# Kernel tuning notes

Measured on AMD Instinct MI355X. Metric: run time of the kernel, lower is better.

The kernel has to match this reference:

```python
import jax, jax.numpy as jnp
import numpy as np

B, C, H, W = 2, 64, 256, 256
DW = 128          # c * DW_Expand
FFN = 128         # c * FFN_Expand
GRID = 8          # wH = wW modulation grid


def setup_inputs() -> dict:
    key = jax.random.key(0)
    ks = jax.random.split(key, 16)
    rn = lambda k, s, sc=1.0: jax.random.normal(k, s, jnp.float32) * sc
    return {
        "x": rn(ks[0], (B, C, H, W)),
        "w1": rn(ks[1], (DW, C), (2.0 / C) ** 0.5),
        "b1": jnp.zeros((DW,), jnp.float32),
        "w2": rn(ks[2], (DW, 3, 3), (2.0 / 9.0) ** 0.5),
        "b2": jnp.zeros((DW,), jnp.float32),
        "w3": rn(ks[3], (C, DW // 2), (2.0 / (DW // 2)) ** 0.5),
        "b3": jnp.zeros((C,), jnp.float32),
        "sca_w": rn(ks[4], (DW // 2, DW // 2), (1.0 / (DW // 2)) ** 0.5),
        "sca_b": jnp.zeros((DW // 2,), jnp.float32),
        "w4": rn(ks[5], (FFN, C), (2.0 / C) ** 0.5),
        "b4": jnp.zeros((FFN,), jnp.float32),
        "w5": rn(ks[6], (C, FFN // 2), (2.0 / (FFN // 2)) ** 0.5),
        "b5": jnp.zeros((C,), jnp.float32),
        "n1_w": jnp.ones((C,), jnp.float32),
        "n1_b": jnp.zeros((C,), jnp.float32),
        "n2_w": jnp.ones((C,), jnp.float32),
        "n2_b": jnp.zeros((C,), jnp.float32),
        "beta": rn(ks[7], (C,), 0.1),
        "gamma": rn(ks[8], (C,), 0.1),
        "mod1": rn(ks[9], (B, DW, C, GRID, GRID)),
        "mod2": rn(ks[10], (B, DW, GRID, GRID)),
        "mod3": rn(ks[11], (B, C, DW // 2, GRID, GRID)),
        "mod4": rn(ks[12], (B, FFN, C, GRID, GRID)),
        "mod5": rn(ks[13], (B, C, FFN // 2, GRID, GRID)),
    }


def layernorm2d(x, w, b, eps=1e-6):
    # channel-wise LayerNorm per pixel (NAFNet LayerNorm2d)
    mu = jnp.mean(x, axis=1, keepdims=True)
    var = jnp.mean((x - mu) ** 2, axis=1, keepdims=True)
    return (x - mu) / jnp.sqrt(var + eps) * w[None, :, None, None] + b[None, :, None, None]


def conv1x1_modulated(x, wb, bb, mod):
    # wb: [Co,Ci], mod: [B,Co,Ci,wH,wW]; per-patch 1x1 conv with normalized dynamic weights
    w = wb[None, :, :, None, None] * mod                      # [B,Co,Ci,wH,wW]
    w = w / jnp.sqrt(jnp.sum(w * w, axis=2, keepdims=True))   # normalize over Ci (kh*kw==1)
    b_, ci, h, wd = x.shape
    wh, ww = mod.shape[-2:]
    ph, pw = h // wh, wd // ww
    xp = x.reshape(b_, ci, wh, ph, ww, pw)                    # split into patches
    y = jnp.einsum('bocuv,bcupvq->boupvq', w, xp)             # per-patch matmul
    return y.reshape(b_, wb.shape[0], h, wd) + bb[None, :, None, None]


def conv3x3_dw_modulated(x, wb, bb, mod):
    # wb: [C,3,3], mod: [B,C,wH,wW]; per-patch depthwise 3x3, padding 1 across whole image
    w = wb[None, :, :, :, None, None] * mod[:, :, None, None, :, :]  # [B,C,3,3,wH,wW]
    w = w / jnp.sqrt(jnp.sum(w * w, axis=(2, 3), keepdims=True))     # normalize over (ci=1, kh*kw)
    b_, c, h, wd = x.shape
    wh, ww = mod.shape[-2:]
    ph, pw = h // wh, wd // ww
    xpad = jnp.pad(x, ((0, 0), (0, 0), (1, 1), (1, 1)))
    out = jnp.zeros_like(x)
    for dh in range(3):
        for dw_ in range(3):
            xs = xpad[:, :, dh:dh + h, dw_:dw_ + wd].reshape(b_, c, wh, ph, ww, pw)
            wk = w[:, :, dh, dw_, :, :]                        # [B,C,wH,wW]
            out = out + (wk[:, :, :, None, :, None] * xs).reshape(b_, c, h, wd)
    return out + bb[None, :, None, None]


def simple_gate(x):
    a, g = jnp.split(x, 2, axis=1)
    return a * g


def reference(x, w1, b1, w2, b2, w3, b3, sca_w, sca_b, w4, b4, w5, b5,
              n1_w, n1_b, n2_w, n2_b, beta, gamma, mod1, mod2, mod3, mod4, mod5):
    y = layernorm2d(x, n1_w, n1_b)
    y = conv1x1_modulated(y, w1, b1, mod1)
    y = conv3x3_dw_modulated(y, w2, b2, mod2)
    y = simple_gate(y)
    s = jnp.mean(y, axis=(2, 3), keepdims=True)               # SCA: global pool + 1x1
    s = jnp.einsum('oc,bcij->boij', sca_w, s) + sca_b[None, :, None, None]
    y = y * s
    y = conv1x1_modulated(y, w3, b3, mod3)
    y1 = x + y * beta[None, :, None, None]
    z = conv1x1_modulated(layernorm2d(y1, n2_w, n2_b), w4, b4, mod4)
    z = simple_gate(z)
    z = conv1x1_modulated(z, w5, b5, mod5)
    return y1 + z * gamma[None, :, None, None]
```

## Files before the change

kernel.cpp:

```cpp
#include <hip/hip_runtime.h>


typedef __bf16 bf16x8 __attribute__((ext_vector_type(8)));
typedef float f32x4 __attribute__((ext_vector_type(4)));
typedef unsigned short u16x8 __attribute__((ext_vector_type(8)));

__device__ __forceinline__ float b2f(unsigned short u) {
    union { unsigned int i; float f; } x; x.i = ((unsigned int)u) << 16; return x.f;
}
__device__ __forceinline__ unsigned short f2b(float f) {
    union { float f; unsigned int i; } x; x.f = f;
    unsigned int i = x.i;
    return (unsigned short)((i + 0x7FFFu + ((i >> 16) & 1u)) >> 16);
}

__global__ __launch_bounds__(256) void prep_k(
    const float* __restrict__ w1, const float* __restrict__ mod1,
    const float* __restrict__ w3, const float* __restrict__ mod3,
    const float* __restrict__ beta,
    const float* __restrict__ w4, const float* __restrict__ mod4,
    unsigned short* __restrict__ pw1, unsigned short* __restrict__ pw3,
    unsigned short* __restrict__ pw4)
{
    const int tid = threadIdx.x;
    int blk = blockIdx.x;
    const float* w; const float* mod; const float* rows = nullptr;
    unsigned short* out; int NOUT; int rem;
    if (blk < 256)      { w = w1; mod = mod1; out = pw1; NOUT = 128; rem = blk; }
    else if (blk < 384) { w = w3; mod = mod3; out = pw3; NOUT = 64; rem = blk - 256; rows = beta; }
    else                { w = w4; mod = mod4; out = pw4; NOUT = 128; rem = blk - 384; }
    const int b = rem / NOUT, o = rem % NOUT;

    __shared__ float mlds[64 * 68];
    __shared__ float wlsh[64];
    __shared__ float red[4 * 64];
    __shared__ float rs[64];

    const float* mbase = mod + ((size_t)(b * NOUT + o) * 64) * 64;
#pragma unroll
    for (int k = 0; k < 4; ++k) {
        int l = tid + k * 256;
        float4 vv = ((const float4*)mbase)[l];
        int c = l >> 4, q = l & 15;
        *(float4*)&mlds[c * 68 + q * 4] = vv;
    }
    if (tid < 64) wlsh[tid] = w[o * 64 + tid];
    __syncthreads();

    {
        int uv = tid & 63, part = tid >> 6;
        float ss = 0.f;
#pragma unroll
        for (int j = 0; j < 16; ++j) {
            int c = part * 16 + j;
            float t = wlsh[c] * mlds[c * 68 + uv];
            ss += t * t;
        }
        red[part * 64 + uv] = ss;
    }
    __syncthreads();
    if (tid < 64) {
        float tot = red[tid] + red[64 + tid] + red[128 + tid] + red[192 + tid];
        float rv = rows ? rows[o] : 1.f;
        rs[tid] = rsqrtf(fmaxf(tot, 1e-30f)) * rv;
    }
    __syncthreads();

    {
        int uvw = tid >> 2, cp = tid & 3;
        float r = rs[uvw];
        size_t obase = ((size_t)(b * 64 + uvw) * NOUT + o) * 64;
#pragma unroll
        for (int g = 0; g < 2; ++g) {
            u16x8 pk;
#pragma unroll
            for (int e = 0; e < 8; ++e) {
                int c = cp * 16 + g * 8 + e;
                pk[e] = f2b(wlsh[c] * mlds[c * 68 + uvw] * r);
            }
            *(u16x8*)&out[obase + cp * 16 + g * 8] = pk;
        }
    }
}

template <int NOUT, bool LN, bool GATE, bool RESID, bool SCALE_IN,
          bool IN_F32, bool RES_F32, bool OUT_F32, bool PREPPED>
__global__ __launch_bounds__(256, 2) void conv_k(
    const void* __restrict__ in_,
    void* __restrict__ out_,
    const unsigned short* __restrict__ pw,
    const float* __restrict__ wb,
    const float* __restrict__ mod,
    const float* __restrict__ bias,
    const float* __restrict__ lnw,
    const float* __restrict__ lnb,
    const void* __restrict__ resid_,
    const float* __restrict__ rows,
    const float* __restrict__ svec,
    int bbase)
{
    constexpr int CHOUT = GATE ? 64 : NOUT;
    constexpr int PARTS = 256 / NOUT;
    constexpr int CP    = 64 / PARTS;

    const int tid   = threadIdx.x;
    const int chunk = blockIdx.x;
    const int uv    = blockIdx.y;
    const int z     = blockIdx.z;
    const int bfull = z + bbase;
    const int u = uv >> 3, v = uv & 7;
    const int h_base = u * 32 + chunk * 4;
    const int w_base = v * 32;

    __shared__ __align__(16) unsigned short stage[128 * 72];
    __shared__ __align__(16) unsigned short wlds[NOUT * 72];
    __shared__ float sbias[NOUT];
    __shared__ float shP[PREPPED ? 1 : 256];
    __shared__ float shsA[LN ? 256 : 1];
    __shared__ float shsB[LN ? 256 : 1];

    const int o_p  = tid & (NOUT - 1);
    const int part = tid / NOUT;
    float wv[PREPPED ? 1 : CP];

    if constexpr (PREPPED) {
        constexpr int CH = NOUT / 32;
        const unsigned short* pwb = pw + ((size_t)(bfull * 64 + uv) * NOUT) * 64;
#pragma unroll
        for (int k = 0; k < CH; ++k) {
            int ci = tid + k * 256;
            *(u16x8*)&wlds[(ci >> 3) * 72 + (ci & 7) * 8] = *(const u16x8*)&pwb[ci * 8];
        }
        if (tid < NOUT) {
            float bs = bias[tid];
            if constexpr (RESID) bs *= rows[tid];
            sbias[tid] = bs;
        }
    } else {
        float ss = 0.f;
#pragma unroll
        for (int j = 0; j < CP; ++j) {
            int c = part * CP + j;
            float wf = wb[o_p * 64 + c];
            float m  = mod[(((bfull * NOUT + o_p) * 64 + c) << 6) + uv];
            wv[j] = wf * m;
            ss += wv[j] * wv[j];
        }
        shP[o_p * PARTS + part] = ss;
    }

    const int p    = tid & 127;
    const int half = tid >> 7;
    const int cbase = half * 32;
    const int pixoff = (h_base + (p >> 5)) * 256 + w_base + (p & 31);
    float v2[32];
    {
        float s1 = 0.f, s2 = 0.f;
#pragma unroll
        for (int j = 0; j < 32; ++j) {
            int idx = ((z * 64 + cbase + j) << 16) + pixoff;
            float xv = IN_F32 ? ((const float*)in_)[idx]
                              : b2f(((const unsigned short*)in_)[idx]);
            v2[j] = xv;
            if constexpr (LN) { s1 += xv; s2 += xv * xv; }
        }
        if constexpr (LN) { shsA[p * 2 + half] = s1; shsB[p * 2 + half] = s2; }
    }

    if constexpr (!LN) {
#pragma unroll
        for (int g = 0; g < 4; ++g) {
            u16x8 pk;
#pragma unroll
            for (int e = 0; e < 8; ++e) {
                int j = g * 8 + e;
                float val = v2[j];
                if constexpr (SCALE_IN) val *= svec[bfull * 64 + cbase + j];
                pk[e] = f2b(val);
            }
            *(u16x8*)&stage[p * 72 + cbase + g * 8] = pk;
        }
    }

    if constexpr (LN || !PREPPED) __syncthreads();

    if constexpr (!PREPPED) {
        float tot = 0.f;
#pragma unroll
        for (int k = 0; k < PARTS; ++k) tot += shP[o_p * PARTS + k];
        float rn = rsqrtf(fmaxf(tot, 1e-30f));
        float rsv = 1.f;
        if constexpr (RESID) { rsv = rows[o_p]; rn *= rsv; }
#pragma unroll
        for (int j = 0; j < CP; ++j)
            wlds[o_p * 72 + part * CP + j] = f2b(wv[j] * rn);
        if (part == 0) {
            float bs = bias[o_p];
            if constexpr (RESID) bs *= rsv;
            sbias[o_p] = bs;
        }
    }

    if constexpr (LN) {
        float S1 = shsA[p * 2] + shsA[p * 2 + 1];
        float S2 = shsB[p * 2] + shsB[p * 2 + 1];
        float mu = S1 * (1.f / 64.f);
        float var = S2 * (1.f / 64.f) - mu * mu;
        float rstd = rsqrtf(fmaxf(var, 0.f) + 1e-6f);
#pragma unroll
        for (int g = 0; g < 4; ++g) {
            u16x8 pk;
#pragma unroll
            for (int e = 0; e < 8; ++e) {
                int j = g * 8 + e;
                float val = (v2[j] - mu) * rstd * lnw[cbase + j] + lnb[cbase + j];
                pk[e] = f2b(val);
            }
            *(u16x8*)&stage[p * 72 + cbase + g * 8] = pk;
        }
    }

    __syncthreads();

    const int wave = tid >> 6;
    const int lane = tid & 63;
    const int q = lane >> 4;
    const int r = lane & 15;

    constexpr int NF = (NOUT == 64) ? 1 : 2;
    int nfi[2];
    if constexpr (NOUT == 64)      { nfi[0] = wave;     nfi[1] = wave; }
    else if constexpr (GATE)       { nfi[0] = wave;     nfi[1] = wave + 4; }
    else                           { nfi[0] = 2 * wave; nfi[1] = 2 * wave + 1; }

    bf16x8 bfr[NF][2];
#pragma unroll
    for (int f = 0; f < NF; ++f)
#pragma unroll
        for (int ks = 0; ks < 2; ++ks)
            bfr[f][ks] = *(const bf16x8*)&wlds[(16 * nfi[f] + r) * 72 + ks * 32 + q * 8];

    f32x4 acc[8][NF];
#pragma unroll
    for (int mi = 0; mi < 8; ++mi)
#pragma unroll
        for (int f = 0; f < NF; ++f) acc[mi][f] = (f32x4){0.f, 0.f, 0.f, 0.f};

#pragma unroll
    for (int mi = 0; mi < 8; ++mi) {
        bf16x8 a0 = *(const bf16x8*)&stage[(16 * mi + r) * 72 + q * 8];
        bf16x8 a1 = *(const bf16x8*)&stage[(16 * mi + r) * 72 + 32 + q * 8];
#pragma unroll
        for (int f = 0; f < NF; ++f) {
            acc[mi][f] = __builtin_amdgcn_mfma_f32_16x16x32_bf16(a0, bfr[f][0], acc[mi][f], 0, 0, 0);
            acc[mi][f] = __builtin_amdgcn_mfma_f32_16x16x32_bf16(a1, bfr[f][1], acc[mi][f], 0, 0, 0);
        }
    }

#pragma unroll
    for (int mi = 0; mi < 8; ++mi) {
        int lp0 = 16 * mi + 4 * q;
        int pix = (h_base + (lp0 >> 5)) * 256 + w_base + (lp0 & 31);
        if constexpr (GATE) {
            int o = 16 * wave + r;
            float ba = sbias[o], bg = sbias[o + 64];
            float g0 = (acc[mi][0][0] + ba) * (acc[mi][1][0] + bg);
            float g1 = (acc[mi][0][1] + ba) * (acc[mi][1][1] + bg);
            float g2 = (acc[mi][0][2] + ba) * (acc[mi][1][2] + bg);
            float g3 = (acc[mi][0][3] + ba) * (acc[mi][1][3] + bg);
            int off = ((z * 64 + o) << 16) + pix;
            *(ushort4*)&((unsigned short*)out_)[off] =
                make_ushort4(f2b(g0), f2b(g1), f2b(g2), f2b(g3));
        } else {
#pragma unroll
            for (int f = 0; f < NF; ++f) {
                int o = 16 * nfi[f] + r;
                float bs = sbias[o];
                float e0 = acc[mi][f][0] + bs, e1 = acc[mi][f][1] + bs;
                float e2 = acc[mi][f][2] + bs, e3 = acc[mi][f][3] + bs;
                int off = ((z * CHOUT + o) << 16) + pix;
                if constexpr (RESID) {
                    if constexpr (RES_F32) {
                        float4 rv = *(const float4*)&((const float*)resid_)[off];
                        e0 += rv.x; e1 += rv.y; e2 += rv.z; e3 += rv.w;
                    } else {
                        ushort4 rv = *(const ushort4*)&((const unsigned short*)resid_)[off];
                        e0 += b2f(rv.x); e1 += b2f(rv.y); e2 += b2f(rv.z); e3 += b2f(rv.w);
                    }
                }
                if constexpr (OUT_F32) {
                    *(float4*)&((float*)out_)[off] = make_float4(e0, e1, e2, e3);
                } else {
                    *(ushort4*)&((unsigned short*)out_)[off] =
                        make_ushort4(f2b(e0), f2b(e1), f2b(e2), f2b(e3));
                }
            }
        }
    }
}

__global__ __launch_bounds__(256, 4) void dw_k(
    const unsigned short* __restrict__ t1,
    unsigned short* __restrict__ t3,
    const float* __restrict__ w2,
    const float* __restrict__ b2,
    const float* __restrict__ mod2,
    float* __restrict__ s0,
    int bbase)
{
    const int tid  = threadIdx.x;
    const int band = blockIdx.x;
    const int oc   = blockIdx.y;
    const int z    = blockIdx.z;
    const int bfull = z + bbase;
    const int u = band >> 2;

    __shared__ float wl[2][8][9];
    __shared__ float wred[4];

    if (tid < 16) {
        int halfc = tid >> 3, vv = tid & 7;
        const float* wrow = w2 + (oc + halfc * 64) * 9;
        float wloc[9], ssum = 0.f;
#pragma unroll
        for (int k = 0; k < 9; ++k) { wloc[k] = wrow[k]; ssum += wloc[k] * wloc[k]; }
        float m = mod2[(bfull * 128 + oc + halfc * 64) * 64 + u * 8 + vv];
        float rn = m * rsqrtf(fmaxf(m * m * ssum, 1e-30f));
#pragma unroll
        for (int k = 0; k < 9; ++k) wl[halfc][vv][k] = wloc[k] * rn;
    }
    __syncthreads();

    const int strip = tid & 31;
    const int row   = band * 8 + (tid >> 5);
    const int v     = strip >> 2;

    float wa[9], wg[9];
#pragma unroll
    for (int k = 0; k < 9; ++k) { wa[k] = wl[0][v][k]; wg[k] = wl[1][v][k]; }
    const float ba = b2[oc], bg = b2[oc + 64];

    const unsigned short* pa = t1 + (((size_t)z * 128 + oc) << 16);
    const unsigned short* pg = pa + ((size_t)64 << 16);

    float fa[3][8], fg[3][8], la[3], ra[3], lg[3], rg[3];
#pragma unroll
    for (int dr = 0; dr < 3; ++dr) {
        int rr = row - 1 + dr;
        if (rr >= 0 && rr < 256) {
            u16x8 va = *(const u16x8*)&pa[rr * 256 + strip * 8];
            u16x8 vg = *(const u16x8*)&pg[rr * 256 + strip * 8];
#pragma unroll
            for (int e = 0; e < 8; ++e) { fa[dr][e] = b2f(va[e]); fg[dr][e] = b2f(vg[e]); }
        } else {
#pragma unroll
            for (int e = 0; e < 8; ++e) { fa[dr][e] = 0.f; fg[dr][e] = 0.f; }
        }
        float t;
        t = __shfl_up(fa[dr][7], 1);   la[dr] = (strip == 0)  ? 0.f : t;
        t = __shfl_up(fg[dr][7], 1);   lg[dr] = (strip == 0)  ? 0.f : t;
        t = __shfl_down(fa[dr][0], 1); ra[dr] = (strip == 31) ? 0.f : t;
        t = __shfl_down(fg[dr][0], 1); rg[dr] = (strip == 31) ? 0.f : t;
    }

    float psum = 0.f;
    u16x8 pk;
#pragma unroll
    for (int j = 0; j < 8; ++j) {
        float a = 0.f, g = 0.f;
#pragma unroll
        for (int dr = 0; dr < 3; ++dr) {
            float m1a = (j == 0) ? la[dr] : fa[dr][j - 1];
            float p1a = (j == 7) ? ra[dr] : fa[dr][j + 1];
            float m1g = (j == 0) ? lg[dr] : fg[dr][j - 1];
            float p1g = (j == 7) ? rg[dr] : fg[dr][j + 1];
            a += wa[dr * 3] * m1a + wa[dr * 3 + 1] * fa[dr][j] + wa[dr * 3 + 2] * p1a;
            g += wg[dr * 3] * m1g + wg[dr * 3 + 1] * fg[dr][j] + wg[dr * 3 + 2] * p1g;
        }
        float val = (a + ba) * (g + bg);
        psum += val;
        pk[j] = f2b(val);
    }
    *(u16x8*)&t3[(((size_t)z * 64 + oc) << 16) + row * 256 + strip * 8] = pk;

    for (int off = 32; off > 0; off >>= 1) psum += __shfl_down(psum, off, 64);
    if ((tid & 63) == 0) wred[tid >> 6] = psum;
    __syncthreads();
    if (tid == 0)
        atomicAdd(&s0[bfull * 64 + oc], wred[0] + wred[1] + wred[2] + wred[3]);
}

__global__ void sca_k(const float* __restrict__ s0,
                      const float* __restrict__ scaw,
                      const float* __restrict__ scab,
                      float* __restrict__ sfin)
{
    int t = threadIdx.x;
    int b = t >> 6, o = t & 63;
    float acc = 0.f;
#pragma unroll 8
    for (int c = 0; c < 64; ++c)
        acc += scaw[o * 64 + c] * s0[b * 64 + c];
    sfin[b * 64 + o] = acc * (1.f / 65536.f) + scab[o];
}

extern "C" void kernel_launch(void* const* d_in, const int* in_sizes, int n_in,
                              void* d_out, int out_size, void* d_ws, size_t ws_size,
                              hipStream_t stream) {
    (void)in_sizes; (void)n_in; (void)out_size;
    const float* x    = (const float*)d_in[0];
    const float* w1   = (const float*)d_in[1];
    const float* b1   = (const float*)d_in[2];
    const float* w2   = (const float*)d_in[3];
    const float* b2   = (const float*)d_in[4];
    const float* w3   = (const float*)d_in[5];
    const float* b3   = (const float*)d_in[6];
    const float* scaw = (const float*)d_in[7];
    const float* scab = (const float*)d_in[8];
    const float* w4   = (const float*)d_in[9];
    const float* b4   = (const float*)d_in[10];
    const float* w5   = (const float*)d_in[11];
    const float* b5   = (const float*)d_in[12];
    const float* n1w  = (const float*)d_in[13];
    const float* n1b  = (const float*)d_in[14];
    const float* n2w  = (const float*)d_in[15];
    const float* n2b  = (const float*)d_in[16];
    const float* beta = (const float*)d_in[17];
    const float* gam  = (const float*)d_in[18];
    const float* mod1 = (const float*)d_in[19];
    const float* mod2 = (const float*)d_in[20];
    const float* mod3 = (const float*)d_in[21];
    const float* mod4 = (const float*)d_in[22];
    const float* mod5 = (const float*)d_in[23];

    char* ws = (char*)d_ws;
    float* outf = (float*)d_out;

    const size_t IMGel = (size_t)64 * 65536;
    const size_t T1B   = (size_t)128 * 65536 * 2;

    const size_t OUTBYTES = 2 * IMGel * 4;
    const size_t PWB1 = 2097152, PWB3 = 1048576, PWB4 = 2097152;
    char* pwbase = (char*)d_out + OUTBYTES - (PWB1 + PWB3 + PWB4);
    unsigned short* pw1 = (unsigned short*)pwbase;
    unsigned short* pw3 = (unsigned short*)(pwbase + PWB1);
    unsigned short* pw4 = (unsigned short*)(pwbase + PWB1 + PWB3);

    const size_t needA = 2 * T1B + 2048;
    const bool planA = ws_size >= needA;

    dim3 blk(256);

    if (planA) {
        unsigned short* t1 = (unsigned short*)ws;
        unsigned short* y1 = (unsigned short*)ws;
        unsigned short* t4 = (unsigned short*)(ws + 2 * IMGel * 2);
        unsigned short* t3 = (unsigned short*)d_out;
        char* statb = ws + 2 * T1B;
        float* s0   = (float*)statb;
        float* sfin = (float*)(statb + 512);

        hipMemsetAsync(s0, 0, 512, stream);
        prep_k<<<640, blk, 0, stream>>>(w1, mod1, w3, mod3, beta, w4, mod4,
                                        pw1, pw3, pw4);
        dim3 gconv(8, 64, 2), gdw(32, 64, 2);

        conv_k<128, true, false, false, false, true, false, false, true>
            <<<gconv, blk, 0, stream>>>(x, t1, pw1, nullptr, nullptr, b1,
                                        n1w, n1b, nullptr, nullptr, nullptr, 0);
        dw_k<<<gdw, blk, 0, stream>>>(t1, t3, w2, b2, mod2, s0, 0);
        sca_k<<<1, 128, 0, stream>>>(s0, scaw, scab, sfin);
        conv_k<64, false, false, true, true, false, true, false, true>
            <<<gconv, blk, 0, stream>>>(t3, y1, pw3, nullptr, nullptr, b3,
                                        nullptr, nullptr, x, beta, sfin, 0);
        conv_k<128, true, true, false, false, false, false, false, true>
            <<<gconv, blk, 0, stream>>>(y1, t4, pw4, nullptr, nullptr, b4,
                                        n2w, n2b, nullptr, nullptr, nullptr, 0);
        conv_k<64, false, false, true, false, false, false, true, false>
            <<<gconv, blk, 0, stream>>>(t4, outf, nullptr, w5, mod5, b5,
                                        nullptr, nullptr, y1, gam, nullptr, 0);
    } else {
        char* statb = ws + T1B;
        float* s0   = (float*)statb;
        float* sfin = (float*)(statb + 512);
        hipMemsetAsync(s0, 0, 512, stream);
        prep_k<<<640, blk, 0, stream>>>(w1, mod1, w3, mod3, beta, w4, mod4,
                                        pw1, pw3, pw4);

        for (int bb = 0; bb < 2; ++bb) {
            const float* x_b   = x    + (size_t)bb * IMGel;
            float*       out_b = outf + (size_t)bb * IMGel;
            const float* mod5_b = mod5;

            unsigned short* t1 = (unsigned short*)ws;
            unsigned short* y1 = (unsigned short*)ws;
            unsigned short* t4 = (unsigned short*)(ws + IMGel * 2);
            unsigned short* t3 = (unsigned short*)out_b;

            dim3 gconv(8, 64, 1), gdw(32, 64, 1);

            conv_k<128, true, false, false, false, true, false, false, true>
                <<<gconv, blk, 0, stream>>>(x_b, t1, pw1, nullptr, nullptr, b1,
                                            n1w, n1b, nullptr, nullptr, nullptr, bb);
            dw_k<<<gdw, blk, 0, stream>>>(t1, t3, w2, b2, mod2, s0, bb);
            sca_k<<<1, 128, 0, stream>>>(s0, scaw, scab, sfin);
            conv_k<64, false, false, true, true, false, true, false, true>
                <<<gconv, blk, 0, stream>>>(t3, y1, pw3, nullptr, nullptr, b3,
                                            nullptr, nullptr, x_b, beta, sfin, bb);
            conv_k<128, true, true, false, false, false, false, false, true>
                <<<gconv, blk, 0, stream>>>(y1, t4, pw4, nullptr, nullptr, b4,
                                            n2w, n2b, nullptr, nullptr, nullptr, bb);
            conv_k<64, false, false, true, false, false, false, true, false>
                <<<gconv, blk, 0, stream>>>(t4, out_b, nullptr, w5, mod5_b, b5,
                                            nullptr, nullptr, y1, gam, nullptr, bb);
        }
    }
}
```

Before: 240.9 us.

## Vectorize conv input loads with shuffle LayerNorm and precompute conv5 weights

Each conv block now loads inputs as float4/ushort4 across four adjacent pixels and eight channels per thread. LayerNorm statistics are reduced with wave shuffles instead of a shared-memory pass, which removes one barrier. The prep kernel also normalizes the conv5 modulated weights into a workspace buffer when space allows, so the last conv reads prepped bf16 weights instead of rebuilding them from mod5 per block. bf16 packing now uses the hardware float2-to-bfloat162 conversion. In exchange the code adds workspace-size branches and changes the smem staging pattern, which may cause bank conflicts.

```diff
diff --git a/kernel.cpp b/kernel.cpp
--- a/kernel.cpp
+++ b/kernel.cpp
@@ -1,4 +1,5 @@
 #include <hip/hip_runtime.h>
+#include <hip/hip_bf16.h>
 
 
 typedef __bf16 bf16x8 __attribute__((ext_vector_type(8)));
@@ -12,6 +13,10 @@
     union { float f; unsigned int i; } x; x.f = f;
     unsigned int i = x.i;
     return (unsigned short)((i + 0x7FFFu + ((i >> 16) & 1u)) >> 16);
+}
+__device__ __forceinline__ unsigned int pk2(float a, float b) {
+    __hip_bfloat162 h = __float22bfloat162_rn(float2{a, b});
+    union { __hip_bfloat162 h; unsigned int u; } cv; cv.h = h; return cv.u;
 }
 
 __global__ __launch_bounds__(256) void prep_k(
@@ -19,16 +24,20 @@
     const float* __restrict__ w3, const float* __restrict__ mod3,
     const float* __restrict__ beta,
     const float* __restrict__ w4, const float* __restrict__ mod4,
+    const float* __restrict__ w5, const float* __restrict__ mod5,
+    const float* __restrict__ gam,
     unsigned short* __restrict__ pw1, unsigned short* __restrict__ pw3,
-    unsigned short* __restrict__ pw4)
+    unsigned short* __restrict__ pw4, unsigned short* __restrict__ pw5)
 {
     const int tid = threadIdx.x;
     int blk = blockIdx.x;
     const float* w; const float* mod; const float* rows = nullptr;
     unsigned short* out; int NOUT; int rem;
     if (blk < 256)      { w = w1; mod = mod1; out = pw1; NOUT = 128; rem = blk; }
-    else if (blk < 384) { w = w3; mod = mod3; out = pw3; NOUT = 64; rem = blk - 256; rows = beta; }
-    else                { w = w4; mod = mod4; out = pw4; NOUT = 128; rem = blk - 384; }
+    else if (blk < 384) { w = w3; mod = mod3; out = pw3; NOUT = 64;  rem = blk - 256; rows = beta; }
+    else if (blk < 640) { w = w4; mod = mod4; out = pw4; NOUT = 128; rem = blk - 384; }
+    else                { w = w5; mod = mod5; out = pw5; NOUT = 64;  rem = blk - 640; rows = gam;
+                          if (out == nullptr) return; }
     const int b = rem / NOUT, o = rem % NOUT;
 
     __shared__ float mlds[64 * 68];
@@ -116,18 +125,14 @@
     __shared__ __align__(16) unsigned short wlds[NOUT * 72];
     __shared__ float sbias[NOUT];
     __shared__ float shP[PREPPED ? 1 : 256];
-    __shared__ float shsA[LN ? 256 : 1];
-    __shared__ float shsB[LN ? 256 : 1];
 
     const int o_p  = tid & (NOUT - 1);
     const int part = tid / NOUT;
     float wv[PREPPED ? 1 : CP];
-
     if constexpr (PREPPED) {
-        constexpr int CH = NOUT / 32;
         const unsigned short* pwb = pw + ((size_t)(bfull * 64 + uv) * NOUT) * 64;
 #pragma unroll
-        for (int k = 0; k < CH; ++k) {
+        for (int k = 0; k < NOUT / 32; ++k) {
             int ci = tid + k * 256;
             *(u16x8*)&wlds[(ci >> 3) * 72 + (ci & 7) * 8] = *(const u16x8*)&pwb[ci * 8];
         }
@@ -141,48 +146,73 @@
 #pragma unroll
         for (int j = 0; j < CP; ++j) {
             int c = part * CP + j;
-            float wf = wb[o_p * 64 + c];
-            float m  = mod[(((bfull * NOUT + o_p) * 64 + c) << 6) + uv];
-            wv[j] = wf * m;
+            wv[j] = wb[o_p * 64 + c] * mod[(((bfull * NOUT + o_p) * 64 + c) << 6) + uv];
             ss += wv[j] * wv[j];
         }
         shP[o_p * PARTS + part] = ss;
     }
 
-    const int p    = tid & 127;
-    const int half = tid >> 7;
-    const int cbase = half * 32;
-    const int pixoff = (h_base + (p >> 5)) * 256 + w_base + (p & 31);
-    float v2[32];
-    {
-        float s1 = 0.f, s2 = 0.f;
-#pragma unroll
-        for (int j = 0; j < 32; ++j) {
-            int idx = ((z * 64 + cbase + j) << 16) + pixoff;
-            float xv = IN_F32 ? ((const float*)in_)[idx]
-                              : b2f(((const unsigned short*)in_)[idx]);
-            v2[j] = xv;
-            if constexpr (LN) { s1 += xv; s2 += xv * xv; }
-        }
-        if constexpr (LN) { shsA[p * 2 + half] = s1; shsB[p * 2 + half] = s2; }
-    }
-
-    if constexpr (!LN) {
-#pragma unroll
-        for (int g = 0; g < 4; ++g) {
-            u16x8 pk;
-#pragma unroll
-            for (int e = 0; e < 8; ++e) {
-                int j = g * 8 + e;
-                float val = v2[j];
-                if constexpr (SCALE_IN) val *= svec[bfull * 64 + cbase + j];
-                pk[e] = f2b(val);
+    const int cg = tid & 7;
+    const int qd = tid >> 3;
+    const int c0 = cg * 8;
+    const int pixg = (h_base + (qd >> 3)) * 256 + w_base + (qd & 7) * 4;
+    float v2[8][4];
+#pragma unroll
+    for (int k = 0; k < 8; ++k) {
+        int idx = ((z * 64 + c0 + k) << 16) + pixg;
+        if constexpr (IN_F32) {
+            float4 t = *(const float4*)&((const float*)in_)[idx];
+            v2[k][0] = t.x; v2[k][1] = t.y; v2[k][2] = t.z; v2[k][3] = t.w;
+        } else {
+            ushort4 t = *(const ushort4*)&((const unsigned short*)in_)[idx];
+            v2[k][0] = b2f(t.x); v2[k][1] = b2f(t.y); v2[k][2] = b2f(t.z); v2[k][3] = b2f(t.w);
+        }
+    }
+    float mu[4], rstd[4];
+    if constexpr (LN) {
+#pragma unroll
+        for (int e = 0; e < 4; ++e) {
+            float s1 = 0.f, s2 = 0.f;
+#pragma unroll
+            for (int k = 0; k < 8; ++k) { s1 += v2[k][e]; s2 += v2[k][e] * v2[k][e]; }
+#pragma unroll
+            for (int m = 1; m < 8; m <<= 1) {
+                s1 += __shfl_xor(s1, m);
+                s2 += __shfl_xor(s2, m);
             }
-            *(u16x8*)&stage[p * 72 + cbase + g * 8] = pk;
-        }
-    }
-
-    if constexpr (LN || !PREPPED) __syncthreads();
+            mu[e] = s1 * (1.f / 64.f);
+            float var = s2 * (1.f / 64.f) - mu[e] * mu[e];
+            rstd[e] = rsqrtf(fmaxf(var, 0.f) + 1e-6f);
+        }
+    }
+    float lw[8], lb[8], sv[8];
+    if constexpr (LN) {
+        *(float4*)&lw[0] = *(const float4*)&lnw[c0];
+        *(float4*)&lw[4] = *(const float4*)&lnw[c0 + 4];
+        *(float4*)&lb[0] = *(const float4*)&lnb[c0];
+        *(float4*)&lb[4] = *(const float4*)&lnb[c0 + 4];
+    }
+    if constexpr (SCALE_IN) {
+        *(float4*)&sv[0] = *(const float4*)&svec[bfull * 64 + c0];
+        *(float4*)&sv[4] = *(const float4*)&svec[bfull * 64 + c0 + 4];
+    }
+#pragma unroll
+    for (int e = 0; e < 4; ++e) {
+        float o8[8];
+#pragma unroll
+        for (int k = 0; k < 8; ++k) {
+            float val = v2[k][e];
+            if constexpr (LN) val = (val - mu[e]) * rstd[e] * lw[k] + lb[k];
+            if constexpr (SCALE_IN) val *= sv[k];
+            o8[k] = val;
+        }
+        uint4 pk;
+        pk.x = pk2(o8[0], o8[1]); pk.y = pk2(o8[2], o8[3]);
+        pk.z = pk2(o8[4], o8[5]); pk.w = pk2(o8[6], o8[7]);
+        *(uint4*)&stage[(qd * 4 + e) * 72 + c0] = pk;
+    }
+
+    __syncthreads();
 
     if constexpr (!PREPPED) {
         float tot = 0.f;
@@ -199,28 +229,8 @@
             if constexpr (RESID) bs *= rsv;
             sbias[o_p] = bs;
         }
-    }
-
-    if constexpr (LN) {
-        float S1 = shsA[p * 2] + shsA[p * 2 + 1];
-        float S2 = shsB[p * 2] + shsB[p * 2 + 1];
-        float mu = S1 * (1.f / 64.f);
-        float var = S2 * (1.f / 64.f) - mu * mu;
-        float rstd = rsqrtf(fmaxf(var, 0.f) + 1e-6f);
-#pragma unroll
-        for (int g = 0; g < 4; ++g) {
-            u16x8 pk;
-#pragma unroll
-            for (int e = 0; e < 8; ++e) {
-                int j = g * 8 + e;
-                float val = (v2[j] - mu) * rstd * lnw[cbase + j] + lnb[cbase + j];
-                pk[e] = f2b(val);
-            }
-            *(u16x8*)&stage[p * 72 + cbase + g * 8] = pk;
-        }
-    }
-
-    __syncthreads();
+        __syncthreads();
+    }
 
     const int wave = tid >> 6;
     const int lane = tid & 63;
@@ -269,8 +279,8 @@
             float g2 = (acc[mi][0][2] + ba) * (acc[mi][1][2] + bg);
             float g3 = (acc[mi][0][3] + ba) * (acc[mi][1][3] + bg);
             int off = ((z * 64 + o) << 16) + pix;
-            *(ushort4*)&((unsigned short*)out_)[off] =
-                make_ushort4(f2b(g0), f2b(g1), f2b(g2), f2b(g3));
+            *(uint2*)&((unsigned short*)out_)[off] =
+                make_uint2((unsigned)pk2(g0, g1), (unsigned)pk2(g2, g3));
         } else {
 #pragma unroll
             for (int f = 0; f < NF; ++f) {
@@ -291,8 +301,8 @@
                 if constexpr (OUT_F32) {
                     *(float4*)&((float*)out_)[off] = make_float4(e0, e1, e2, e3);
                 } else {
-                    *(ushort4*)&((unsigned short*)out_)[off] =
-                        make_ushort4(f2b(e0), f2b(e1), f2b(e2), f2b(e3));
+                    *(uint2*)&((unsigned short*)out_)[off] =
+                        make_uint2((unsigned)pk2(e0, e1), (unsigned)pk2(e2, e3));
                 }
             }
         }
@@ -440,29 +450,33 @@
     const size_t T1B   = (size_t)128 * 65536 * 2;
 
     const size_t OUTBYTES = 2 * IMGel * 4;
-    const size_t PWB1 = 2097152, PWB3 = 1048576, PWB4 = 2097152;
+    const size_t PWB1 = 2097152, PWB3 = 1048576, PWB4 = 2097152, PWB5 = 1048576;
     char* pwbase = (char*)d_out + OUTBYTES - (PWB1 + PWB3 + PWB4);
     unsigned short* pw1 = (unsigned short*)pwbase;
     unsigned short* pw3 = (unsigned short*)(pwbase + PWB1);
     unsigned short* pw4 = (unsigned short*)(pwbase + PWB1 + PWB3);
 
-    const size_t needA = 2 * T1B + 2048;
+    const size_t needA = 2 * T1B + 4096;
     const bool planA = ws_size >= needA;
+    const size_t NBT = planA ? 2 : 1;
+    const bool havePw5 = ws_size >= NBT * T1B + 4096 + PWB5;
+    char* statb = ws + NBT * T1B;
+    float* s0   = (float*)statb;
+    float* sfin = (float*)(statb + 512);
+    unsigned short* pw5 = havePw5 ? (unsigned short*)(statb + 4096) : nullptr;
 
     dim3 blk(256);
+
+    hipMemsetAsync(s0, 0, 512, stream);
+    prep_k<<<768, blk, 0, stream>>>(w1, mod1, w3, mod3, beta, w4, mod4,
+                                    w5, mod5, gam, pw1, pw3, pw4, pw5);
 
     if (planA) {
         unsigned short* t1 = (unsigned short*)ws;
         unsigned short* y1 = (unsigned short*)ws;
         unsigned short* t4 = (unsigned short*)(ws + 2 * IMGel * 2);
         unsigned short* t3 = (unsigned short*)d_out;
-        char* statb = ws + 2 * T1B;
-        float* s0   = (float*)statb;
-        float* sfin = (float*)(statb + 512);
-
-        hipMemsetAsync(s0, 0, 512, stream);
-        prep_k<<<640, blk, 0, stream>>>(w1, mod1, w3, mod3, beta, w4, mod4,
-                                        pw1, pw3, pw4);
+
         dim3 gconv(8, 64, 2), gdw(32, 64, 2);
 
         conv_k<128, true, false, false, false, true, false, false, true>
@@ -476,21 +490,19 @@
         conv_k<128, true, true, false, false, false, false, false, true>
             <<<gconv, blk, 0, stream>>>(y1, t4, pw4, nullptr, nullptr, b4,
                                         n2w, n2b, nullptr, nullptr, nullptr, 0);
-        conv_k<64, false, false, true, false, false, false, true, false>
-            <<<gconv, blk, 0, stream>>>(t4, outf, nullptr, w5, mod5, b5,
-                                        nullptr, nullptr, y1, gam, nullptr, 0);
+        if (havePw5) {
+            conv_k<64, false, false, true, false, false, false, true, true>
+                <<<gconv, blk, 0, stream>>>(t4, outf, pw5, nullptr, nullptr, b5,
+                                            nullptr, nullptr, y1, gam, nullptr, 0);
+        } else {
+            conv_k<64, false, false, true, false, false, false, true, false>
+                <<<gconv, blk, 0, stream>>>(t4, outf, nullptr, w5, mod5, b5,
+                                            nullptr, nullptr, y1, gam, nullptr, 0);
+        }
     } else {
-        char* statb = ws + T1B;
-        float* s0   = (float*)statb;
-        float* sfin = (float*)(statb + 512);
-        hipMemsetAsync(s0, 0, 512, stream);
-        prep_k<<<640, blk, 0, stream>>>(w1, mod1, w3, mod3, beta, w4, mod4,
-                                        pw1, pw3, pw4);
-
         for (int bb = 0; bb < 2; ++bb) {
             const float* x_b   = x    + (size_t)bb * IMGel;
             float*       out_b = outf + (size_t)bb * IMGel;
-            const float* mod5_b = mod5;
 
             unsigned short* t1 = (unsigned short*)ws;
             unsigned short* y1 = (unsigned short*)ws;
@@ -510,9 +522,15 @@
             conv_k<128, true, true, false, false, false, false, false, true>
                 <<<gconv, blk, 0, stream>>>(y1, t4, pw4, nullptr, nullptr, b4,
                                             n2w, n2b, nullptr, nullptr, nullptr, bb);
-            conv_k<64, false, false, true, false, false, false, true, false>
-                <<<gconv, blk, 0, stream>>>(t4, out_b, nullptr, w5, mod5_b, b5,
-                                            nullptr, nullptr, y1, gam, nullptr, bb);
-        }
-    }
-}
+            if (havePw5) {
+                conv_k<64, false, false, true, false, false, false, true, true>
+                    <<<gconv, blk, 0, stream>>>(t4, out_b, pw5, nullptr, nullptr, b5,
+                                                nullptr, nullptr, y1, gam, nullptr, bb);
+            } else {
+                conv_k<64, false, false, true, false, false, false, true, false>
+                    <<<gconv, blk, 0, stream>>>(t4, out_b, nullptr, w5, mod5, b5,
+                                                nullptr, nullptr, y1, gam, nullptr, bb);
+            }
+        }
+    }
+}
```

After: 225.7 us. -6.3%, faster.
